# Performance work log

Hardware: AMD Instinct MI355X
Metric: run time of the kernel (lower is better)

The kernel has to match this reference:

```python
import jax, jax.numpy as jnp
import numpy as np

B = 65536      # batch
DIM = 32       # flow dimension
NH = 24        # hidden width of each per-dim MLP
PARITY = False # order = reversed(range(dim)) when parity is False
NEG_SLOPE = 0.2


def _causal_mask(dim, dtype):
    # mask[k, j] = 1 if j <= k ; stacked layer k corresponds to torch layer i=k+1
    # which sees x[:, :i] = columns 0..k
    return (jnp.arange(dim)[None, :] <= jnp.arange(dim - 1)[:, None]).astype(dtype)


def setup_inputs() -> dict:
    key = jax.random.key(0)
    ks = jax.random.split(key, 10)
    s = 0.1
    x = jax.random.normal(ks[0], (B, DIM), jnp.float32)
    p0 = jax.random.normal(ks[1], (2,), jnp.float32) * s          # LeafParam(2)
    W1 = jax.random.normal(ks[2], (DIM - 1, NH, DIM), jnp.float32) * s
    W1 = W1 * _causal_mask(DIM, jnp.float32)[:, None, :]          # zero padded cols j > k
    b1 = jax.random.normal(ks[3], (DIM - 1, NH), jnp.float32) * s
    W2 = jax.random.normal(ks[4], (DIM - 1, NH, NH), jnp.float32) * s
    b2 = jax.random.normal(ks[5], (DIM - 1, NH), jnp.float32) * s
    W3 = jax.random.normal(ks[6], (DIM - 1, NH, NH), jnp.float32) * s
    b3 = jax.random.normal(ks[7], (DIM - 1, NH), jnp.float32) * s
    W4 = jax.random.normal(ks[8], (DIM - 1, 2, NH), jnp.float32) * s
    b4 = jax.random.normal(ks[9], (DIM - 1, 2), jnp.float32) * s
    return {"x": x, "p0": p0, "W1": W1, "b1": b1, "W2": W2, "b2": b2,
            "W3": W3, "b3": b3, "W4": W4, "b4": b4}


def reference(x, p0, W1, b1, W2, b2, W3, b3, W4, b4):
    # SlowMAF.forward: per-dim MLP(x[:, :i]) -> (s, t); z[:, order[i]] = x[:, i]*exp(s)+t
    # All dim-1 tiny MLPs are fused into stacked batched GEMMs; the growing slice
    # x[:, :i] is realized via a causal mask on the first-layer weights (same math).
    Bsz, dim = x.shape
    lrelu = lambda h: jnp.where(h > 0, h, NEG_SLOPE * h)  # LeakyReLU(0.2)
    W1m = W1 * _causal_mask(dim, x.dtype)[:, None, :]
    h = lrelu(jnp.einsum('bd,khd->bkh', x, W1m) + b1)      # (B, dim-1, NH)
    h = lrelu(jnp.einsum('bkh,kHh->bkH', h, W2) + b2)
    h = lrelu(jnp.einsum('bkh,kHh->bkH', h, W3) + b3)
    st = jnp.einsum('bkh,koh->bko', h, W4) + b4            # (B, dim-1, 2)
    st0 = jnp.broadcast_to(p0[None, None, :], (Bsz, 1, 2)) # LeafParam for dim 0
    st_all = jnp.concatenate([st0, st], axis=1)            # (B, dim, 2)
    s = st_all[..., 0]
    t = st_all[..., 1]
    vals = x * jnp.exp(s) + t                              # (B, dim)
    order = jnp.arange(dim) if PARITY else jnp.arange(dim)[::-1]
    z = jnp.zeros_like(x).at[:, order].set(vals)
    log_det = jnp.sum(s, axis=1)                           # (B,)
    return z, log_det
```

## Files before the change

### kernel.cpp

```cpp
#include <hip/hip_runtime.h>
#include <hip/hip_bf16.h>

#define BATCH 65536
#define DIM 32
#define NEG 0.2f

typedef short    sfrag8 __attribute__((ext_vector_type(8)));
typedef float    f32x16 __attribute__((ext_vector_type(16)));
typedef unsigned u32x4  __attribute__((ext_vector_type(4)));

__device__ __forceinline__ short f2bf(float v) {
    __bf16 b = (__bf16)v;
    return __builtin_bit_cast(short, b);
}

__device__ __forceinline__ unsigned pack2bf(float v0, float v1) {
    unsigned lo = (unsigned short)f2bf(v0);
    unsigned hi = (unsigned short)f2bf(v1);
    return lo | (hi << 16);
}

__device__ float frag_elem(int k, int f, int r, int h, int j,
    const float* W1, const float* b1, const float* W2, const float* b2,
    const float* W3, const float* b3, const float* W4, const float* b4)
{
    if (f == 0) return (r < 24) ? W1[k*768 + r*32 + 8*h + j] : 0.f;
    if (f == 1) {
        if (r >= 24) return 0.f;
        int c = 16 + 8*h + j;
        if (c == 31) return b1[k*24 + r];
        return W1[k*768 + r*32 + c];
    }
    const float* W; const float* bb; int R;
    if (f < 4)      { W = W2 + k*576; bb = b2 + k*24; R = 24; }
    else if (f < 6) { W = W3 + k*576; bb = b3 + k*24; R = 24; }
    else            { W = W4 + k*48;  bb = b4 + k*2;  R = 2;  }
    if (r >= R) return 0.f;
    if ((f & 1) == 0) {
        int feat = j + 4*h + (j >= 4 ? 4 : 0);
        return W[r*24 + feat];
    } else {
        if (j < 4)            return W[r*24 + 16 + 4*h + j];
        if (j == 4 && h == 0) return bb[r];
        return 0.f;
    }
}

__global__ __launch_bounds__(256) void prep_frags(
    const float* __restrict__ W1, const float* __restrict__ b1,
    const float* __restrict__ W2, const float* __restrict__ b2,
    const float* __restrict__ W3, const float* __restrict__ b3,
    const float* __restrict__ W4, const float* __restrict__ b4,
    short* __restrict__ wsf)
{
    int t = blockIdx.x * 256 + threadIdx.x;
    int lane = t & 63, f = (t >> 6) & 7, k = t >> 9;
    int r = lane & 31, h = lane >> 5;
    sfrag8 o;
    #pragma unroll
    for (int j = 0; j < 8; j++)
        o[j] = f2bf(frag_elem(k, f, r, h, j, W1, b1, W2, b2, W3, b3, W4, b4));
    *(sfrag8*)(wsf + (size_t)t * 8) = o;
}

__device__ __forceinline__ void transition(const f32x16 a, unsigned c1,
                                           sfrag8& blo, sfrag8& bhi)
{
    unsigned P[6];
    #pragma unroll
    for (int g = 0; g < 6; g++) {
        float v0 = a[2*g], v1 = a[2*g + 1];
        v0 = fmaxf(v0, NEG * v0);
        v1 = fmaxf(v1, NEG * v1);
        P[g] = pack2bf(v0, v1);
    }
    blo = __builtin_bit_cast(sfrag8, (u32x4){P[0], P[1], P[2], P[3]});
    bhi = __builtin_bit_cast(sfrag8, (u32x4){P[4], P[5], c1, 0u});
}

template<bool PREPPED>
__global__ __launch_bounds__(256) void maf2(
    const float* __restrict__ x, const float* __restrict__ p0,
    const float* __restrict__ W1, const float* __restrict__ b1,
    const float* __restrict__ W2, const float* __restrict__ b2,
    const float* __restrict__ W3, const float* __restrict__ b3,
    const float* __restrict__ W4, const float* __restrict__ b4,
    const short* __restrict__ wsf,
    float* __restrict__ out)
{
    const int  kg   = blockIdx.y;
    const int  lane = threadIdx.x & 63;
    const int  wave = threadIdx.x >> 6;
    const bool hi   = lane >= 32;
    const int  h    = hi ? 1 : 0;
    const int  r    = lane & 31;
    const int  k0   = kg ? 4*kg - 1 : 0;
    const int  nk   = kg ? 4 : 3;
    const int  c0   = 28 - 4*kg;
    const int  colbase = (blockIdx.x * 4 + wave) * 64;
    const unsigned c1 = hi ? 0u : 0x3F80u;

    sfrag8 xlo[2], xhi[2];
    float  xa[2][4];
    #pragma unroll
    for (int t = 0; t < 2; t++) {
        const float* xp = x + (size_t)(colbase + t*32 + r) * DIM;
        float4 q0 = *(const float4*)(xp + 8*h);
        float4 q1 = *(const float4*)(xp + 8*h + 4);
        float4 q2 = *(const float4*)(xp + 16 + 8*h);
        float4 q3 = *(const float4*)(xp + 16 + 8*h + 4);
        sfrag8 lo, hh;
        lo[0]=f2bf(q0.x); lo[1]=f2bf(q0.y); lo[2]=f2bf(q0.z); lo[3]=f2bf(q0.w);
        lo[4]=f2bf(q1.x); lo[5]=f2bf(q1.y); lo[6]=f2bf(q1.z); lo[7]=f2bf(q1.w);
        hh[0]=f2bf(q2.x); hh[1]=f2bf(q2.y); hh[2]=f2bf(q2.z); hh[3]=f2bf(q2.w);
        hh[4]=f2bf(q3.x); hh[5]=f2bf(q3.y); hh[6]=f2bf(q3.z);
        hh[7] = hi ? f2bf(1.0f) : f2bf(q3.w);
        xlo[t] = lo; xhi[t] = hh;
        float4 qa = *(const float4*)(xp + 4*kg);
        xa[t][0] = qa.x; xa[t][1] = qa.y; xa[t][2] = qa.z; xa[t][3] = qa.w;
    }

    f32x16 Z;
    #pragma unroll
    for (int q = 0; q < 16; q++) Z[q] = 0.f;

    float za[2][4];
    float ld[2] = {0.f, 0.f};

    #pragma unroll
    for (int i = 0; i < 4; i++) {
        if (i < nk) {
            int k = k0 + i;
            sfrag8 F[8];
            if (PREPPED) {
                const short* fp = wsf + ((size_t)k * 512 + lane) * 8;
                #pragma unroll
                for (int f = 0; f < 8; f++) F[f] = *(const sfrag8*)(fp + f * 512);
            } else {
                #pragma unroll
                for (int f = 0; f < 8; f++)
                    #pragma unroll
                    for (int j = 0; j < 8; j++)
                        F[f][j] = f2bf(frag_elem(k, f, r, h, j,
                                                 W1, b1, W2, b2, W3, b3, W4, b4));
            }

            f32x16 acc[2];
            sfrag8 blo[2], bh2[2];
            #pragma unroll
            for (int t = 0; t < 2; t++) {
                f32x16 a = __builtin_amdgcn_mfma_f32_32x32x16_bf16(F[0], xlo[t], Z, 0, 0, 0);
                acc[t]   = __builtin_amdgcn_mfma_f32_32x32x16_bf16(F[1], xhi[t], a, 0, 0, 0);
            }
            #pragma unroll
            for (int t = 0; t < 2; t++) transition(acc[t], c1, blo[t], bh2[t]);
            #pragma unroll
            for (int t = 0; t < 2; t++) {
                f32x16 a = __builtin_amdgcn_mfma_f32_32x32x16_bf16(F[2], blo[t], Z, 0, 0, 0);
                acc[t]   = __builtin_amdgcn_mfma_f32_32x32x16_bf16(F[3], bh2[t], a, 0, 0, 0);
            }
            #pragma unroll
            for (int t = 0; t < 2; t++) transition(acc[t], c1, blo[t], bh2[t]);
            #pragma unroll
            for (int t = 0; t < 2; t++) {
                f32x16 a = __builtin_amdgcn_mfma_f32_32x32x16_bf16(F[4], blo[t], Z, 0, 0, 0);
                acc[t]   = __builtin_amdgcn_mfma_f32_32x32x16_bf16(F[5], bh2[t], a, 0, 0, 0);
            }
            #pragma unroll
            for (int t = 0; t < 2; t++) transition(acc[t], c1, blo[t], bh2[t]);
            #pragma unroll
            for (int t = 0; t < 2; t++) {
                f32x16 a = __builtin_amdgcn_mfma_f32_32x32x16_bf16(F[6], blo[t], Z, 0, 0, 0);
                acc[t]   = __builtin_amdgcn_mfma_f32_32x32x16_bf16(F[7], bh2[t], a, 0, 0, 0);
            }

            #pragma unroll
            for (int t = 0; t < 2; t++) {
                float s  = acc[t][0];
                float tt = acc[t][1];
                float e  = __expf(s);
                if (kg) { za[t][3 - i] = xa[t][i] * e + tt; }
                else if (i < 3) { za[t][2 - i] = xa[t][i + 1] * e + tt; }
                ld[t] += s;
            }
        }
    }

    if (kg == 0) {
        float s0 = p0[0], t0 = p0[1];
        float e0 = __expf(s0);
        #pragma unroll
        for (int t = 0; t < 2; t++) {
            za[t][3] = xa[t][0] * e0 + t0;
            ld[t] += s0;
        }
    }

    if (!hi) {
        #pragma unroll
        for (int t = 0; t < 2; t++) {
            int b = colbase + t*32 + r;
            float4 v; v.x = za[t][0]; v.y = za[t][1]; v.z = za[t][2]; v.w = za[t][3];
            *(float4*)(out + (size_t)b * DIM + c0) = v;
            atomicAdd(out + (size_t)BATCH * DIM + b, ld[t]);
        }
    }
}

extern "C" void kernel_launch(void* const* d_in, const int* in_sizes, int n_in,
                              void* d_out, int out_size, void* d_ws, size_t ws_size,
                              hipStream_t stream)
{
    const float* x  = (const float*)d_in[0];
    const float* p0 = (const float*)d_in[1];
    const float* W1 = (const float*)d_in[2];
    const float* b1 = (const float*)d_in[3];
    const float* W2 = (const float*)d_in[4];
    const float* b2 = (const float*)d_in[5];
    const float* W3 = (const float*)d_in[6];
    const float* b3 = (const float*)d_in[7];
    const float* W4 = (const float*)d_in[8];
    const float* b4 = (const float*)d_in[9];
    float* out = (float*)d_out;

    const size_t FRG = (size_t)31 * 8 * 64 * 8;
    if (ws_size >= FRG * sizeof(short)) {
        short* wsf = (short*)d_ws;
        prep_frags<<<62, 256, 0, stream>>>(W1, b1, W2, b2, W3, b3, W4, b4, wsf);
        maf2<true><<<dim3(256, 8), 256, 0, stream>>>(
            x, p0, W1, b1, W2, b2, W3, b3, W4, b4, wsf, out);
    } else {
        maf2<false><<<dim3(256, 8), 256, 0, stream>>>(
            x, p0, W1, b1, W2, b2, W3, b3, W4, b4, nullptr, out);
    }
}
```

Measured before the change: 115.0 us.

## Switch MFMA path to fp16 with packed LeakyReLU and one tile per wave

Replaces the bf16 MFMA operands with fp16 and uses packed round-toward-zero conversion plus packed half max/mul for the LeakyReLU transitions, which cuts per-element conversion and ALU work. Each wave now handles 32 batch rows instead of 64, so the grid doubles and launch bounds request 4 blocks per SM to raise occupancy. In exchange each wave loses interleaving of two independent MFMA chains per weight fragment load, so weight fragment loads per output double. fp16 also has less range than bf16, which is risky if activations grow large.

```diff
diff --git a/kernel.cpp b/kernel.cpp
--- a/kernel.cpp
+++ b/kernel.cpp
@@ -1,23 +1,26 @@
 #include <hip/hip_runtime.h>
-#include <hip/hip_bf16.h>
 
 #define BATCH 65536
 #define DIM 32
 #define NEG 0.2f
 
 typedef short    sfrag8 __attribute__((ext_vector_type(8)));
+typedef _Float16 hfrag8 __attribute__((ext_vector_type(8)));
+typedef _Float16 h2     __attribute__((ext_vector_type(2)));
 typedef float    f32x16 __attribute__((ext_vector_type(16)));
 typedef unsigned u32x4  __attribute__((ext_vector_type(4)));
 
-__device__ __forceinline__ short f2bf(float v) {
-    __bf16 b = (__bf16)v;
-    return __builtin_bit_cast(short, b);
-}
-
-__device__ __forceinline__ unsigned pack2bf(float v0, float v1) {
-    unsigned lo = (unsigned short)f2bf(v0);
-    unsigned hi = (unsigned short)f2bf(v1);
-    return lo | (hi << 16);
+__device__ __forceinline__ short f2h(float v) {
+    _Float16 h = (_Float16)v;
+    return __builtin_bit_cast(short, h);
+}
+
+__device__ __forceinline__ h2 cvt2h(float a, float b) {
+    return __builtin_bit_cast(h2, __builtin_amdgcn_cvt_pkrtz(a, b));
+}
+
+__device__ __forceinline__ unsigned pack2h(float a, float b) {
+    return __builtin_bit_cast(unsigned, __builtin_amdgcn_cvt_pkrtz(a, b));
 }
 
 __device__ float frag_elem(int k, int f, int r, int h, int j,
@@ -59,27 +62,27 @@
     sfrag8 o;
     #pragma unroll
     for (int j = 0; j < 8; j++)
-        o[j] = f2bf(frag_elem(k, f, r, h, j, W1, b1, W2, b2, W3, b3, W4, b4));
+        o[j] = f2h(frag_elem(k, f, r, h, j, W1, b1, W2, b2, W3, b3, W4, b4));
     *(sfrag8*)(wsf + (size_t)t * 8) = o;
 }
 
 __device__ __forceinline__ void transition(const f32x16 a, unsigned c1,
-                                           sfrag8& blo, sfrag8& bhi)
-{
+                                           hfrag8& blo, hfrag8& bhi)
+{
+    const h2 s02 = {(_Float16)0.2f, (_Float16)0.2f};
     unsigned P[6];
     #pragma unroll
     for (int g = 0; g < 6; g++) {
-        float v0 = a[2*g], v1 = a[2*g + 1];
-        v0 = fmaxf(v0, NEG * v0);
-        v1 = fmaxf(v1, NEG * v1);
-        P[g] = pack2bf(v0, v1);
-    }
-    blo = __builtin_bit_cast(sfrag8, (u32x4){P[0], P[1], P[2], P[3]});
-    bhi = __builtin_bit_cast(sfrag8, (u32x4){P[4], P[5], c1, 0u});
+        h2 v = cvt2h(a[2*g], a[2*g + 1]);
+        h2 r = __builtin_elementwise_max(v, v * s02);
+        P[g] = __builtin_bit_cast(unsigned, r);
+    }
+    blo = __builtin_bit_cast(hfrag8, (u32x4){P[0], P[1], P[2], P[3]});
+    bhi = __builtin_bit_cast(hfrag8, (u32x4){P[4], P[5], c1, 0u});
 }
 
 template<bool PREPPED>
-__global__ __launch_bounds__(256) void maf2(
+__global__ __launch_bounds__(256, 4) void maf2(
     const float* __restrict__ x, const float* __restrict__ p0,
     const float* __restrict__ W1, const float* __restrict__ b1,
     const float* __restrict__ W2, const float* __restrict__ b2,
@@ -97,113 +100,83 @@
     const int  k0   = kg ? 4*kg - 1 : 0;
     const int  nk   = kg ? 4 : 3;
     const int  c0   = 28 - 4*kg;
-    const int  colbase = (blockIdx.x * 4 + wave) * 64;
-    const unsigned c1 = hi ? 0u : 0x3F80u;
-
-    sfrag8 xlo[2], xhi[2];
-    float  xa[2][4];
-    #pragma unroll
-    for (int t = 0; t < 2; t++) {
-        const float* xp = x + (size_t)(colbase + t*32 + r) * DIM;
-        float4 q0 = *(const float4*)(xp + 8*h);
-        float4 q1 = *(const float4*)(xp + 8*h + 4);
-        float4 q2 = *(const float4*)(xp + 16 + 8*h);
-        float4 q3 = *(const float4*)(xp + 16 + 8*h + 4);
-        sfrag8 lo, hh;
-        lo[0]=f2bf(q0.x); lo[1]=f2bf(q0.y); lo[2]=f2bf(q0.z); lo[3]=f2bf(q0.w);
-        lo[4]=f2bf(q1.x); lo[5]=f2bf(q1.y); lo[6]=f2bf(q1.z); lo[7]=f2bf(q1.w);
-        hh[0]=f2bf(q2.x); hh[1]=f2bf(q2.y); hh[2]=f2bf(q2.z); hh[3]=f2bf(q2.w);
-        hh[4]=f2bf(q3.x); hh[5]=f2bf(q3.y); hh[6]=f2bf(q3.z);
-        hh[7] = hi ? f2bf(1.0f) : f2bf(q3.w);
-        xlo[t] = lo; xhi[t] = hh;
-        float4 qa = *(const float4*)(xp + 4*kg);
-        xa[t][0] = qa.x; xa[t][1] = qa.y; xa[t][2] = qa.z; xa[t][3] = qa.w;
-    }
+    const int  col  = (blockIdx.x * 4 + wave) * 32 + r;
+    const unsigned c1 = hi ? 0u : 0x3C00u;
+
+    const float* xp = x + (size_t)col * DIM;
+    float4 q0 = *(const float4*)(xp + 8*h);
+    float4 q1 = *(const float4*)(xp + 8*h + 4);
+    float4 q2 = *(const float4*)(xp + 16 + 8*h);
+    float4 q3 = *(const float4*)(xp + 16 + 8*h + 4);
+    unsigned L0 = pack2h(q0.x, q0.y), L1 = pack2h(q0.z, q0.w);
+    unsigned L2 = pack2h(q1.x, q1.y), L3 = pack2h(q1.z, q1.w);
+    unsigned H0 = pack2h(q2.x, q2.y), H1 = pack2h(q2.z, q2.w);
+    unsigned H2 = pack2h(q3.x, q3.y);
+    unsigned H3 = pack2h(q3.z, hi ? 1.0f : q3.w);
+    hfrag8 xlo = __builtin_bit_cast(hfrag8, (u32x4){L0, L1, L2, L3});
+    hfrag8 xhi = __builtin_bit_cast(hfrag8, (u32x4){H0, H1, H2, H3});
+
+    float4 qa = *(const float4*)(xp + 4*kg);
+    float xa[4] = {qa.x, qa.y, qa.z, qa.w};
 
     f32x16 Z;
     #pragma unroll
     for (int q = 0; q < 16; q++) Z[q] = 0.f;
 
-    float za[2][4];
-    float ld[2] = {0.f, 0.f};
+    float za[4];
+    float ld = 0.f;
 
     #pragma unroll
     for (int i = 0; i < 4; i++) {
         if (i < nk) {
             int k = k0 + i;
-            sfrag8 F[8];
+            hfrag8 F[8];
             if (PREPPED) {
                 const short* fp = wsf + ((size_t)k * 512 + lane) * 8;
                 #pragma unroll
-                for (int f = 0; f < 8; f++) F[f] = *(const sfrag8*)(fp + f * 512);
+                for (int f = 0; f < 8; f++) F[f] = *(const hfrag8*)(fp + f * 512);
             } else {
                 #pragma unroll
                 for (int f = 0; f < 8; f++)
                     #pragma unroll
                     for (int j = 0; j < 8; j++)
-                        F[f][j] = f2bf(frag_elem(k, f, r, h, j,
-                                                 W1, b1, W2, b2, W3, b3, W4, b4));
+                        F[f][j] = (_Float16)frag_elem(k, f, r, h, j,
+                                                      W1, b1, W2, b2, W3, b3, W4, b4);
             }
 
-            f32x16 acc[2];
-            sfrag8 blo[2], bh2[2];
-            #pragma unroll
-            for (int t = 0; t < 2; t++) {
-                f32x16 a = __builtin_amdgcn_mfma_f32_32x32x16_bf16(F[0], xlo[t], Z, 0, 0, 0);
-                acc[t]   = __builtin_amdgcn_mfma_f32_32x32x16_bf16(F[1], xhi[t], a, 0, 0, 0);
-            }
-            #pragma unroll
-            for (int t = 0; t < 2; t++) transition(acc[t], c1, blo[t], bh2[t]);
-            #pragma unroll
-            for (int t = 0; t < 2; t++) {
-                f32x16 a = __builtin_amdgcn_mfma_f32_32x32x16_bf16(F[2], blo[t], Z, 0, 0, 0);
-                acc[t]   = __builtin_amdgcn_mfma_f32_32x32x16_bf16(F[3], bh2[t], a, 0, 0, 0);
-            }
-            #pragma unroll
-            for (int t = 0; t < 2; t++) transition(acc[t], c1, blo[t], bh2[t]);
-            #pragma unroll
-            for (int t = 0; t < 2; t++) {
-                f32x16 a = __builtin_amdgcn_mfma_f32_32x32x16_bf16(F[4], blo[t], Z, 0, 0, 0);
-                acc[t]   = __builtin_amdgcn_mfma_f32_32x32x16_bf16(F[5], bh2[t], a, 0, 0, 0);
-            }
-            #pragma unroll
-            for (int t = 0; t < 2; t++) transition(acc[t], c1, blo[t], bh2[t]);
-            #pragma unroll
-            for (int t = 0; t < 2; t++) {
-                f32x16 a = __builtin_amdgcn_mfma_f32_32x32x16_bf16(F[6], blo[t], Z, 0, 0, 0);
-                acc[t]   = __builtin_amdgcn_mfma_f32_32x32x16_bf16(F[7], bh2[t], a, 0, 0, 0);
-            }
-
-            #pragma unroll
-            for (int t = 0; t < 2; t++) {
-                float s  = acc[t][0];
-                float tt = acc[t][1];
-                float e  = __expf(s);
-                if (kg) { za[t][3 - i] = xa[t][i] * e + tt; }
-                else if (i < 3) { za[t][2 - i] = xa[t][i + 1] * e + tt; }
-                ld[t] += s;
-            }
+            f32x16 a1  = __builtin_amdgcn_mfma_f32_32x32x16_f16(F[0], xlo, Z, 0, 0, 0);
+            f32x16 acc = __builtin_amdgcn_mfma_f32_32x32x16_f16(F[1], xhi, a1, 0, 0, 0);
+            hfrag8 blo, bh2;
+            transition(acc, c1, blo, bh2);
+            a1  = __builtin_amdgcn_mfma_f32_32x32x16_f16(F[2], blo, Z, 0, 0, 0);
+            acc = __builtin_amdgcn_mfma_f32_32x32x16_f16(F[3], bh2, a1, 0, 0, 0);
+            transition(acc, c1, blo, bh2);
+            a1  = __builtin_amdgcn_mfma_f32_32x32x16_f16(F[4], blo, Z, 0, 0, 0);
+            acc = __builtin_amdgcn_mfma_f32_32x32x16_f16(F[5], bh2, a1, 0, 0, 0);
+            transition(acc, c1, blo, bh2);
+            a1  = __builtin_amdgcn_mfma_f32_32x32x16_f16(F[6], blo, Z, 0, 0, 0);
+            acc = __builtin_amdgcn_mfma_f32_32x32x16_f16(F[7], bh2, a1, 0, 0, 0);
+
+            float s  = acc[0];
+            float tt = acc[1];
+            float e  = __expf(s);
+            if (kg) { za[3 - i] = xa[i] * e + tt; }
+            else if (i < 3) { za[2 - i] = xa[i + 1] * e + tt; }
+            ld += s;
         }
     }
 
     if (kg == 0) {
         float s0 = p0[0], t0 = p0[1];
         float e0 = __expf(s0);
-        #pragma unroll
-        for (int t = 0; t < 2; t++) {
-            za[t][3] = xa[t][0] * e0 + t0;
-            ld[t] += s0;
-        }
+        za[3] = xa[0] * e0 + t0;
+        ld += s0;
     }
 
     if (!hi) {
-        #pragma unroll
-        for (int t = 0; t < 2; t++) {
-            int b = colbase + t*32 + r;
-            float4 v; v.x = za[t][0]; v.y = za[t][1]; v.z = za[t][2]; v.w = za[t][3];
-            *(float4*)(out + (size_t)b * DIM + c0) = v;
-            atomicAdd(out + (size_t)BATCH * DIM + b, ld[t]);
-        }
+        float4 v; v.x = za[0]; v.y = za[1]; v.z = za[2]; v.w = za[3];
+        *(float4*)(out + (size_t)col * DIM + c0) = v;
+        atomicAdd(out + (size_t)BATCH * DIM + col, ld);
     }
 }
 
@@ -227,10 +200,10 @@
     if (ws_size >= FRG * sizeof(short)) {
         short* wsf = (short*)d_ws;
         prep_frags<<<62, 256, 0, stream>>>(W1, b1, W2, b2, W3, b3, W4, b4, wsf);
-        maf2<true><<<dim3(256, 8), 256, 0, stream>>>(
+        maf2<true><<<dim3(512, 8), 256, 0, stream>>>(
             x, p0, W1, b1, W2, b2, W3, b3, W4, b4, wsf, out);
     } else {
-        maf2<false><<<dim3(256, 8), 256, 0, stream>>>(
+        maf2<false><<<dim3(512, 8), 256, 0, stream>>>(
             x, p0, W1, b1, W2, b2, W3, b3, W4, b4, nullptr, out);
     }
 }
```

Measured after the change: 107.6 us. -6.4%, faster.
